# Performance work log

Hardware: AMD Instinct MI355X
Metric: run time of the kernel (lower is better)

The kernel has to match this reference:

```python
import jax, jax.numpy as jnp
import numpy as np

NUM_HEADS = 8
WS = 2  # window_size


def setup_inputs() -> dict:
    key = jax.random.key(0)
    k1, k2, k3 = jax.random.split(key, 3)
    B, N, C = 8, 4096, 512
    x = jax.random.normal(k1, (B, N, C), dtype=jnp.float32)
    W_qkv = jax.random.normal(k2, (3 * C, C), dtype=jnp.float32) * 0.02  # nn.Linear weight [out,in], no bias
    W_proj = jax.random.normal(k3, (C, C), dtype=jnp.float32) * 0.02
    b_proj = jnp.zeros((C,), dtype=jnp.float32)
    return {"x": x, "W_qkv": W_qkv, "W_proj": W_proj, "b_proj": b_proj}


def _attn(q, k, v, scale):
    # q,k,v: [..., heads, T, hd]
    logits = jnp.einsum('...qd,...kd->...qk', q, k) * scale
    p = jax.nn.softmax(logits, axis=-1)
    return jnp.einsum('...qk,...kd->...qd', p, v)


def reference(x, W_qkv, W_proj, b_proj):
    B, N, C = x.shape
    H = W = int(N ** 0.5)
    nh, hd = NUM_HEADS, C // NUM_HEADS
    scale = hd ** -0.5

    # ---- hi branch: avg-pool then global attention on pooled tokens ----
    x_img = x.reshape(B, H, W, C)
    x_hi = x_img.reshape(B, H // WS, WS, W // WS, WS, C).mean(axis=(2, 4))  # [B,Hh,Wh,C]
    Hh, Wh = H // WS, W // WS
    N_hi = Hh * Wh
    x_hi = x_hi.reshape(B, N_hi, C)

    qkv_hi = (x_hi @ W_qkv.T).reshape(B, N_hi, 3, nh, hd).transpose(2, 0, 3, 1, 4)
    out_hi = _attn(qkv_hi[0], qkv_hi[1], qkv_hi[2], scale)          # [B,nh,N_hi,hd]
    out_hi = out_hi.transpose(0, 2, 1, 3).reshape(B, N_hi, C)

    # bilinear upsample (align_corners=False == half-pixel, matches jax.image.resize)
    hi_img = out_hi.reshape(B, Hh, Wh, C).transpose(0, 3, 1, 2)      # [B,C,Hh,Wh]
    hi_up = jax.image.resize(hi_img, (B, C, H, W), method='bilinear')
    out_hi = hi_up.reshape(B, C, N).transpose(0, 2, 1)               # [B,N,C]

    # ---- lo branch: windowed attention (replicating torch unfold layout) ----
    # torch: x.unfold(1,ws,ws).unfold(2,ws,ws) -> [B,Hh,Wh,C,ws,ws]; then
    # .reshape(B,-1,ws*ws,C) reinterprets the contiguous [C,ws,ws] block as [ws*ws,C].
    wnd = x_img.reshape(B, Hh, WS, Wh, WS, C).transpose(0, 1, 3, 5, 2, 4)  # [B,Hh,Wh,C,ws,ws]
    nW = Hh * Wh
    T = WS * WS
    windows = wnd.reshape(B, nW, T, C)  # same raw-memory reinterpretation as torch

    qkv_lo = (windows @ W_qkv.T).reshape(B, nW, T, 3, nh, hd).transpose(3, 0, 1, 4, 2, 5)
    out_lo = _attn(qkv_lo[0], qkv_lo[1], qkv_lo[2], scale)           # [B,nW,nh,T,hd]
    out_lo = out_lo.transpose(0, 1, 3, 2, 4).reshape(B, nW, T, C)

    out_lo = out_lo.reshape(B, Hh, Wh, WS, WS, C).transpose(0, 1, 3, 2, 4, 5).reshape(B, N, C)

    out = out_hi + out_lo
    out = out @ W_proj.T + b_proj
    return out
```

## Files before the change

kernel.cpp:

```cpp
#include <hip/hip_runtime.h>
#include <stdint.h>

typedef unsigned short u16b;
typedef short s16x8 __attribute__((ext_vector_type(8)));
typedef unsigned short u16x4 __attribute__((ext_vector_type(4)));
typedef float f32x4 __attribute__((ext_vector_type(4)));

__device__ __forceinline__ u16b f2bf(float f) {
    uint32_t u = __float_as_uint(f);
    uint32_t r = (u + 0x7FFFu + ((u >> 16) & 1u)) >> 16;
    return (u16b)r;
}
__device__ __forceinline__ u16b f2bf_fast(float f) {
    return (u16b)((__float_as_uint(f) + 0x8000u) >> 16);
}
__device__ __forceinline__ float bf2f(u16b h) {
    return __uint_as_float(((uint32_t)h) << 16);
}

typedef const __attribute__((address_space(1))) void* gas_ptr;
typedef __attribute__((address_space(3))) void* las_ptr;
__device__ __forceinline__ void gload_lds16(const void* g, void* l) {
    __builtin_amdgcn_global_load_lds((gas_ptr)g, (las_ptr)l, 16, 0, 0);
}

__global__ void cast_weights(const float* __restrict__ wqkv, const float* __restrict__ wproj,
                             u16b* __restrict__ wqkv_bf, u16b* __restrict__ wproj_bf) {
    int i = blockIdx.x * 256 + threadIdx.x;
    if (i < 1536 * 512) wqkv_bf[i] = f2bf(wqkv[i]);
    if (i < 512 * 512) wproj_bf[i] = f2bf(wproj[i]);
}

__global__ __launch_bounds__(256) void pool_pack(const float* __restrict__ x,
                                                 u16b* __restrict__ x_hi,
                                                 u16b* __restrict__ xw) {
    int i = blockIdx.x * 256 + threadIdx.x;
    int c4 = i & 127;
    int t = i >> 7;
    int wj = t & 31, wi = (t >> 5) & 31, b = t >> 10;
    const float* p00 = x + ((size_t)b * 4096 + (size_t)(wi * 2) * 64 + wj * 2) * 512 + c4 * 4;
    f32x4 v00 = *(const f32x4*)p00;
    f32x4 v01 = *(const f32x4*)(p00 + 512);
    f32x4 v10 = *(const f32x4*)(p00 + 64 * 512);
    f32x4 v11 = *(const f32x4*)(p00 + 65 * 512);

    u16b ph[4];
#pragma unroll
    for (int j = 0; j < 4; ++j)
        ph[j] = f2bf((v00[j] + v01[j] + v10[j] + v11[j]) * 0.25f);
    *(u16x4*)(x_hi + (size_t)t * 512 + c4 * 4) = *(u16x4*)ph;

    u16b pk[16];
#pragma unroll
    for (int j = 0; j < 4; ++j) {
        pk[j * 4 + 0] = f2bf(v00[j]);
        pk[j * 4 + 1] = f2bf(v01[j]);
        pk[j * 4 + 2] = f2bf(v10[j]);
        pk[j * 4 + 3] = f2bf(v11[j]);
    }
    u16b* dst = xw + ((size_t)t * 4 + (c4 >> 5)) * 512 + (c4 & 31) * 16;
    *(s16x8*)dst = *(s16x8*)pk;
    *(s16x8*)(dst + 8) = *(s16x8*)(pk + 8);
}


template <int RT>
__device__ __forceinline__ void stage_region(const u16b* gsrc, int K, u16b* lds,
                                             int wv, int ldrow, int ldk) {
#pragma unroll
    for (int j = 0; j < 2; ++j) {
        int c = j * 8 + wv;
        int chunk;
        if (RT == 0)      chunk = c + ((c >> 3) << 3);
        else if (RT == 1) chunk = c + ((c >> 3) << 3) + 8;
        else if (RT == 2) chunk = ((c >> 2) << 3) + (c & 3);
        else              chunk = ((c >> 2) << 3) + (c & 3) + 4;
        gload_lds16(gsrc + (size_t)(chunk * 8 + ldrow) * K + ldk, lds + chunk * 512);
    }
}

template <int MH, int NH, int LOADB>
__device__ __forceinline__ void ds_quad(const u16b* Asb, const u16b* Bsb,
                                        int gm, int gn, int l15, int fsw0, int fsw1,
                                        s16x8 (&af)[4][2], s16x8 (&bf)[2][2]) {
#pragma unroll
    for (int i = 0; i < 4; ++i) {
        const u16b* p = Asb + (gm * 128 + (MH * 4 + i) * 16 + l15) * 64;
        af[i][0] = *(const s16x8*)(p + fsw0);
        af[i][1] = *(const s16x8*)(p + fsw1);
    }
    if (LOADB) {
#pragma unroll
        for (int i = 0; i < 2; ++i) {
            const u16b* p = Bsb + (gn * 64 + (NH * 2 + i) * 16 + l15) * 64;
            bf[i][0] = *(const s16x8*)(p + fsw0);
            bf[i][1] = *(const s16x8*)(p + fsw1);
        }
    }
}

template <int MH, int NH>
__device__ __forceinline__ void mfma_quad(s16x8 (&af)[4][2], s16x8 (&bf)[2][2], f32x4 (&acc)[8][4]) {
    __builtin_amdgcn_s_setprio(1);
#pragma unroll
    for (int ks = 0; ks < 2; ++ks)
#pragma unroll
        for (int i = 0; i < 4; ++i)
#pragma unroll
            for (int j = 0; j < 2; ++j)
                acc[MH * 4 + i][NH * 2 + j] = __builtin_amdgcn_mfma_f32_16x16x32_bf16(
                    af[i][ks], bf[j][ks], acc[MH * 4 + i][NH * 2 + j], 0, 0, 0);
    __builtin_amdgcn_s_setprio(0);
}

template <int OUT_F32>
__global__ __launch_bounds__(512, 2) void gemm8(const u16b* __restrict__ A, const u16b* __restrict__ Bt,
                                                u16b* __restrict__ Cbf, float* __restrict__ Cf,
                                                const float* __restrict__ bias, int M, int Nn, int K,
                                                int NB) {
    __shared__ u16b As[2][256 * 64];
    __shared__ u16b Bs[2][256 * 64];
    int tid = threadIdx.x;
    int wv = tid >> 6, lane = tid & 63;
    int quad = lane >> 4, l15 = lane & 15;
    int gm = wv >> 2, gn = wv & 3;

    int nwg = gridDim.x, bid = blockIdx.x;
    int swz = (bid & 7) * (nwg >> 3) + (bid >> 3);
    int nb = swz % NB, mb = swz / NB;
    int m0 = mb * 256, n0 = nb * 256;
    const u16b* Ap = A + (size_t)m0 * K;
    const u16b* Btp = Bt + (size_t)n0 * K;

    int ldrow = lane >> 3;
    int ldk = ((lane & 7) ^ ldrow) * 8;
    int fsw0 = (quad ^ (l15 & 7)) * 8;
    int fsw1 = ((4 + quad) ^ (l15 & 7)) * 8;

    f32x4 acc[8][4] = {};
    s16x8 af[4][2], bf[2][2];
    int nt = K >> 6;

#pragma unroll
    for (int r = 0; r < 4; ++r) {
        int chunk = r * 8 + wv;
        gload_lds16(Ap + (size_t)(chunk * 8 + ldrow) * K + ldk, &As[0][0] + chunk * 512);
    }
#pragma unroll
    for (int r = 0; r < 4; ++r) {
        int chunk = r * 8 + wv;
        gload_lds16(Btp + (size_t)(chunk * 8 + ldrow) * K + ldk, &Bs[0][0] + chunk * 512);
    }
    stage_region<2>(Btp + 64, K, &Bs[1][0], wv, ldrow, ldk);
    stage_region<0>(Ap + 64, K, &As[1][0], wv, ldrow, ldk);
    asm volatile("s_waitcnt vmcnt(4)" ::: "memory");
    __builtin_amdgcn_s_barrier();

    for (int t0 = 0; t0 < nt; t0 += 2) {
        bool s2 = (t0 + 2) < nt;
        bool s3 = (t0 + 3) < nt;
        ds_quad<0, 0, 1>(&As[0][0], &Bs[0][0], gm, gn, l15, fsw0, fsw1, af, bf);
        stage_region<3>(Btp + (size_t)(t0 + 1) * 64, K, &Bs[1][0], wv, ldrow, ldk);
        __builtin_amdgcn_s_barrier();
        mfma_quad<0, 0>(af, bf, acc);
        __builtin_amdgcn_s_barrier();
        ds_quad<1, 0, 0>(&As[0][0], &Bs[0][0], gm, gn, l15, fsw0, fsw1, af, bf);
        stage_region<1>(Ap + (size_t)(t0 + 1) * 64, K, &As[1][0], wv, ldrow, ldk);
        __builtin_amdgcn_s_barrier();
        mfma_quad<1, 0>(af, bf, acc);
        __builtin_amdgcn_s_barrier();
        ds_quad<0, 1, 1>(&As[0][0], &Bs[0][0], gm, gn, l15, fsw0, fsw1, af, bf);
        if (s2) stage_region<2>(Btp + (size_t)(t0 + 2) * 64, K, &Bs[0][0], wv, ldrow, ldk);
        __builtin_amdgcn_s_barrier();
        mfma_quad<0, 1>(af, bf, acc);
        __builtin_amdgcn_s_barrier();
        ds_quad<1, 1, 0>(&As[0][0], &Bs[0][0], gm, gn, l15, fsw0, fsw1, af, bf);
        if (s2) stage_region<0>(Ap + (size_t)(t0 + 2) * 64, K, &As[0][0], wv, ldrow, ldk);
        __builtin_amdgcn_s_barrier();
        mfma_quad<1, 1>(af, bf, acc);
        if (s2) { asm volatile("s_waitcnt vmcnt(4)" ::: "memory"); }
        else    { asm volatile("s_waitcnt vmcnt(0)" ::: "memory"); }
        __builtin_amdgcn_s_barrier();
        ds_quad<0, 0, 1>(&As[1][0], &Bs[1][0], gm, gn, l15, fsw0, fsw1, af, bf);
        if (s2) stage_region<3>(Btp + (size_t)(t0 + 2) * 64, K, &Bs[0][0], wv, ldrow, ldk);
        __builtin_amdgcn_s_barrier();
        mfma_quad<0, 0>(af, bf, acc);
        __builtin_amdgcn_s_barrier();
        ds_quad<1, 0, 0>(&As[1][0], &Bs[1][0], gm, gn, l15, fsw0, fsw1, af, bf);
        if (s2) stage_region<1>(Ap + (size_t)(t0 + 2) * 64, K, &As[0][0], wv, ldrow, ldk);
        __builtin_amdgcn_s_barrier();
        mfma_quad<1, 0>(af, bf, acc);
        __builtin_amdgcn_s_barrier();
        ds_quad<0, 1, 1>(&As[1][0], &Bs[1][0], gm, gn, l15, fsw0, fsw1, af, bf);
        if (s3) stage_region<2>(Btp + (size_t)(t0 + 3) * 64, K, &Bs[1][0], wv, ldrow, ldk);
        __builtin_amdgcn_s_barrier();
        mfma_quad<0, 1>(af, bf, acc);
        __builtin_amdgcn_s_barrier();
        ds_quad<1, 1, 0>(&As[1][0], &Bs[1][0], gm, gn, l15, fsw0, fsw1, af, bf);
        if (s3) stage_region<0>(Ap + (size_t)(t0 + 3) * 64, K, &As[1][0], wv, ldrow, ldk);
        __builtin_amdgcn_s_barrier();
        mfma_quad<1, 1>(af, bf, acc);
        if (s3) { asm volatile("s_waitcnt vmcnt(4)" ::: "memory"); }
        else    { asm volatile("s_waitcnt vmcnt(0)" ::: "memory"); }
        __builtin_amdgcn_s_barrier();
    }

#pragma unroll
    for (int mi = 0; mi < 8; ++mi)
#pragma unroll
        for (int ni = 0; ni < 4; ++ni) {
            int row = m0 + gm * 128 + mi * 16 + quad * 4;
            int col = n0 + gn * 64 + ni * 16 + l15;
            if (OUT_F32) {
                float bv = bias[col];
#pragma unroll
                for (int r = 0; r < 4; ++r)
                    Cf[(size_t)(row + r) * Nn + col] = acc[mi][ni][r] + bv;
            } else {
#pragma unroll
                for (int r = 0; r < 4; ++r)
                    Cbf[(size_t)(row + r) * Nn + col] = f2bf(acc[mi][ni][r]);
            }
        }
}

__global__ __launch_bounds__(256) void transpose_v(const u16b* __restrict__ qkv, u16b* __restrict__ vt) {
    __shared__ u16b tile[64 * 72];
    int bh = blockIdx.y, nt = blockIdx.x;
    int b = bh >> 3, h = bh & 7;
    int tid = threadIdx.x;
    int row = tid >> 2, part = tid & 3;
    const u16b* src = qkv + ((size_t)b * 1024 + nt * 64 + row) * 1536 + 1024 + h * 64 + part * 16;
    *(s16x8*)&tile[row * 72 + part * 16] = *(const s16x8*)src;
    *(s16x8*)&tile[row * 72 + part * 16 + 8] = *(const s16x8*)(src + 8);
    __syncthreads();
    u16b* dst = vt + ((size_t)bh * 64 + row) * 1024 + nt * 64 + part * 16;
#pragma unroll
    for (int j = 0; j < 16; ++j) dst[j] = tile[(part * 16 + j) * 72 + row];
}

__global__ __launch_bounds__(256) void attn_hi(const u16b* __restrict__ qkv,
                                               const u16b* __restrict__ vt,
                                               u16b* __restrict__ out_hi) {
    __shared__ u16b Ks[2][64 * 64];
    __shared__ u16b Vs[2][64 * 64];
    __shared__ u16b P[4][16 * 64];
    int tid = threadIdx.x, wave = tid >> 6, lane = tid & 63;
    int quad = lane >> 4, l15 = lane & 15;
    int bh = blockIdx.x;
    int qb = blockIdx.y;
    int b = bh >> 3, h = bh & 7;
    int qr0 = qb * 64 + wave * 16;

    const size_t qkv_b = (size_t)b * 1024 * 1536;
    const u16b* kg = qkv + qkv_b + 512 + h * 64;
    const u16b* vg = vt + (size_t)bh * 64 * 1024;

    int srow8 = lane >> 3;
    int ssw = ((lane & 7) ^ srow8) * 8;
    int fsw0 = (quad ^ (l15 & 7)) * 8;
    int fsw1 = ((4 + quad) ^ (l15 & 7)) * 8;

    s16x8 qf[2];
    qf[0] = *(const s16x8*)(qkv + qkv_b + (size_t)(qr0 + l15) * 1536 + h * 64 + quad * 8);
    qf[1] = *(const s16x8*)(qkv + qkv_b + (size_t)(qr0 + l15) * 1536 + h * 64 + 32 + quad * 8);

#pragma unroll
    for (int i = 0; i < 2; ++i) {
        int chunk = wave * 2 + i;
        int row = chunk * 8 + srow8;
        gload_lds16(kg + (size_t)row * 1536 + ssw, (u16b*)Ks[0] + chunk * 512);
        gload_lds16(vg + (size_t)row * 1024 + ssw, (u16b*)Vs[0] + chunk * 512);
    }

    f32x4 o[4] = {};
    f32x4 ls = {0.f, 0.f, 0.f, 0.f};
    u16b* pl = P[wave];
    const float c_scale = 0.18033688011f;

    for (int kb = 0; kb < 16; ++kb) {
        int cur = kb & 1, nxt = cur ^ 1;
        __syncthreads();
        if (kb < 15) {
#pragma unroll
            for (int i = 0; i < 2; ++i) {
                int chunk = wave * 2 + i;
                int row = chunk * 8 + srow8;
                gload_lds16(kg + (size_t)((kb + 1) * 64 + row) * 1536 + ssw, (u16b*)Ks[nxt] + chunk * 512);
                gload_lds16(vg + (size_t)row * 1024 + (kb + 1) * 64 + ssw, (u16b*)Vs[nxt] + chunk * 512);
            }
        }
        const u16b* Kc = Ks[cur];
        const u16b* Vc = Vs[cur];

        f32x4 s[4] = {};
#pragma unroll
        for (int nt = 0; nt < 4; ++nt) {
            s16x8 kf0 = *(const s16x8*)(Kc + (nt * 16 + l15) * 64 + fsw0);
            s16x8 kf1 = *(const s16x8*)(Kc + (nt * 16 + l15) * 64 + fsw1);
            s[nt] = __builtin_amdgcn_mfma_f32_16x16x32_bf16(qf[0], kf0, s[nt], 0, 0, 0);
            s[nt] = __builtin_amdgcn_mfma_f32_16x16x32_bf16(qf[1], kf1, s[nt], 0, 0, 0);
        }
#pragma unroll
        for (int nt = 0; nt < 4; ++nt) {
            f32x4 p;
#pragma unroll
            for (int r = 0; r < 4; ++r) p[r] = exp2f(s[nt][r] * c_scale);
            ls += p;
#pragma unroll
            for (int r = 0; r < 4; ++r) {
                int prow = quad * 4 + r;
                int slc = (nt * 2 + (l15 >> 3)) ^ (prow & 7);
                pl[prow * 64 + slc * 8 + (l15 & 7)] = f2bf_fast(p[r]);
            }
        }
        s16x8 pa0 = *(const s16x8*)(pl + l15 * 64 + fsw0);
        s16x8 pa1 = *(const s16x8*)(pl + l15 * 64 + fsw1);
#pragma unroll
        for (int nd = 0; nd < 4; ++nd) {
            s16x8 vf0 = *(const s16x8*)(Vc + (nd * 16 + l15) * 64 + fsw0);
            s16x8 vf1 = *(const s16x8*)(Vc + (nd * 16 + l15) * 64 + fsw1);
            o[nd] = __builtin_amdgcn_mfma_f32_16x16x32_bf16(pa0, vf0, o[nd], 0, 0, 0);
            o[nd] = __builtin_amdgcn_mfma_f32_16x16x32_bf16(pa1, vf1, o[nd], 0, 0, 0);
        }
    }

    float rs[4];
#pragma unroll
    for (int r = 0; r < 4; ++r) {
        float t = ls[r];
#pragma unroll
        for (int msk = 1; msk < 16; msk <<= 1) t += __shfl_xor(t, msk);
        rs[r] = 1.f / t;
    }
#pragma unroll
    for (int nd = 0; nd < 4; ++nd)
#pragma unroll
        for (int r = 0; r < 4; ++r) {
            int row = qr0 + quad * 4 + r;
            int col = h * 64 + nd * 16 + l15;
            out_hi[((size_t)b * 1024 + row) * 512 + col] = f2bf(o[nd][r] * rs[r]);
        }
}

__global__ __launch_bounds__(256) void attn_lo_up(const u16b* __restrict__ qkv_lo,
                                                  const u16b* __restrict__ out_hi,
                                                  u16b* __restrict__ attn_sum) {
    int tid = threadIdx.x, wave = tid >> 6, lane = tid & 63;
    int wg = blockIdx.x * 4 + wave;
    int h = wg & 7, w = (wg >> 3) & 1023, b = wg >> 13;
    size_t base = ((size_t)(b * 1024 + w) * 4) * 1536 + h * 64 + lane;
    float q[4], k[4], v[4];
#pragma unroll
    for (int t = 0; t < 4; ++t) {
        q[t] = bf2f(qkv_lo[base + t * 1536]);
        k[t] = bf2f(qkv_lo[base + t * 1536 + 512]);
        v[t] = bf2f(qkv_lo[base + t * 1536 + 1024]);
    }
    float lg[4][4];
#pragma unroll
    for (int tq = 0; tq < 4; ++tq)
#pragma unroll
        for (int tk = 0; tk < 4; ++tk) {
            float d = q[tq] * k[tk];
#pragma unroll
            for (int msk = 1; msk < 64; msk <<= 1) d += __shfl_xor(d, msk);
            lg[tq][tk] = d * 0.125f;
        }
    int wi = w >> 5, wj = w & 31;
    const u16b* hsrc = out_hi + (size_t)b * 1024 * 512 + h * 64 + lane;
#pragma unroll
    for (int tq = 0; tq < 4; ++tq) {
        float mx = fmaxf(fmaxf(lg[tq][0], lg[tq][1]), fmaxf(lg[tq][2], lg[tq][3]));
        float p[4], s = 0.f;
#pragma unroll
        for (int tk = 0; tk < 4; ++tk) { p[tk] = exp2f((lg[tq][tk] - mx) * 1.44269504f); s += p[tk]; }
        float ov = 0.f;
#pragma unroll
        for (int tk = 0; tk < 4; ++tk) ov += p[tk] * v[tk];
        ov /= s;
        int py = tq >> 1, px = tq & 1;
        int y0, y1, x0, x1;
        float wy0, wx0;
        if (py == 0) { y0 = wi > 0 ? wi - 1 : 0; y1 = wi; wy0 = 0.25f; }
        else         { y0 = wi; y1 = wi < 31 ? wi + 1 : 31; wy0 = 0.75f; }
        if (px == 0) { x0 = wj > 0 ? wj - 1 : 0; x1 = wj; wx0 = 0.25f; }
        else         { x0 = wj; x1 = wj < 31 ? wj + 1 : 31; wx0 = 0.75f; }
        float wy1 = 1.f - wy0, wx1 = 1.f - wx0;
        float vu = wy0 * (wx0 * bf2f(hsrc[(size_t)(y0 * 32 + x0) * 512]) + wx1 * bf2f(hsrc[(size_t)(y0 * 32 + x1) * 512]))
                 + wy1 * (wx0 * bf2f(hsrc[(size_t)(y1 * 32 + x0) * 512]) + wx1 * bf2f(hsrc[(size_t)(y1 * 32 + x1) * 512]));
        int n = (wi * 2 + py) * 64 + wj * 2 + px;
        attn_sum[((size_t)b * 4096 + n) * 512 + h * 64 + lane] = f2bf(ov + vu);
    }
}

extern "C" void kernel_launch(void* const* d_in, const int* in_sizes, int n_in,
                              void* d_out, int out_size, void* d_ws, size_t ws_size,
                              hipStream_t stream) {
    (void)in_sizes; (void)n_in; (void)out_size; (void)ws_size;
    const float* x = (const float*)d_in[0];
    const float* Wqkv = (const float*)d_in[1];
    const float* Wproj = (const float*)d_in[2];
    const float* bproj = (const float*)d_in[3];
    float* out = (float*)d_out;

    char* ws = (char*)d_ws;
    size_t off = 0;
    auto alloc = [&](size_t bytes) { void* p = ws + off; off += bytes; return p; };
    u16b* wqkv_bf = (u16b*)alloc((size_t)1536 * 512 * 2);
    u16b* wproj_bf = (u16b*)alloc((size_t)512 * 512 * 2);
    u16b* x_hi    = (u16b*)alloc((size_t)8 * 1024 * 512 * 2);
    u16b* xw      = (u16b*)alloc((size_t)8 * 1024 * 4 * 512 * 2);
    u16b* qkv_hi  = (u16b*)alloc((size_t)8 * 1024 * 1536 * 2);
    u16b* qkv_lo  = (u16b*)alloc((size_t)8 * 4096 * 1536 * 2);
    u16b* vt      = (u16b*)alloc((size_t)64 * 64 * 1024 * 2);
    u16b* out_hi  = (u16b*)alloc((size_t)8 * 1024 * 512 * 2);
    u16b* attn_sum= (u16b*)alloc((size_t)8 * 4096 * 512 * 2);

    cast_weights<<<dim3(3072), dim3(256), 0, stream>>>(Wqkv, Wproj, wqkv_bf, wproj_bf);
    pool_pack<<<dim3(4096), dim3(256), 0, stream>>>(x, x_hi, xw);
    gemm8<0><<<dim3(192), dim3(512), 0, stream>>>(x_hi, wqkv_bf, qkv_hi, nullptr, nullptr, 8192, 1536, 512, 6);
    gemm8<0><<<dim3(768), dim3(512), 0, stream>>>(xw, wqkv_bf, qkv_lo, nullptr, nullptr, 32768, 1536, 512, 6);
    transpose_v<<<dim3(16, 64), dim3(256), 0, stream>>>(qkv_hi, vt);
    attn_hi<<<dim3(64, 16), dim3(256), 0, stream>>>(qkv_hi, vt, out_hi);
    attn_lo_up<<<dim3(16384), dim3(256), 0, stream>>>(qkv_lo, out_hi, attn_sum);
    gemm8<1><<<dim3(256), dim3(512), 0, stream>>>(attn_sum, wproj_bf, nullptr, out, bproj, 32768, 512, 512, 2);
}
```

Measured before the change: 356.2 us.

## Use MFMA for windowed attention logits and reorder GEMM quadrant traversal

```diff
diff --git a/kernel.cpp b/kernel.cpp
--- a/kernel.cpp
+++ b/kernel.cpp
@@ -79,17 +79,19 @@
     }
 }
 
-template <int MH, int NH, int LOADB>
+template <int MH, int NH, int LA, int LB>
 __device__ __forceinline__ void ds_quad(const u16b* Asb, const u16b* Bsb,
                                         int gm, int gn, int l15, int fsw0, int fsw1,
                                         s16x8 (&af)[4][2], s16x8 (&bf)[2][2]) {
-#pragma unroll
-    for (int i = 0; i < 4; ++i) {
-        const u16b* p = Asb + (gm * 128 + (MH * 4 + i) * 16 + l15) * 64;
-        af[i][0] = *(const s16x8*)(p + fsw0);
-        af[i][1] = *(const s16x8*)(p + fsw1);
-    }
-    if (LOADB) {
+    if (LA) {
+#pragma unroll
+        for (int i = 0; i < 4; ++i) {
+            const u16b* p = Asb + (gm * 128 + (MH * 4 + i) * 16 + l15) * 64;
+            af[i][0] = *(const s16x8*)(p + fsw0);
+            af[i][1] = *(const s16x8*)(p + fsw1);
+        }
+    }
+    if (LB) {
 #pragma unroll
         for (int i = 0; i < 2; ++i) {
             const u16b* p = Bsb + (gn * 64 + (NH * 2 + i) * 16 + l15) * 64;
@@ -151,55 +153,55 @@
         int chunk = r * 8 + wv;
         gload_lds16(Btp + (size_t)(chunk * 8 + ldrow) * K + ldk, &Bs[0][0] + chunk * 512);
     }
-    stage_region<2>(Btp + 64, K, &Bs[1][0], wv, ldrow, ldk);
     stage_region<0>(Ap + 64, K, &As[1][0], wv, ldrow, ldk);
+    stage_region<3>(Btp + 64, K, &Bs[1][0], wv, ldrow, ldk);
     asm volatile("s_waitcnt vmcnt(4)" ::: "memory");
     __builtin_amdgcn_s_barrier();
 
     for (int t0 = 0; t0 < nt; t0 += 2) {
         bool s2 = (t0 + 2) < nt;
         bool s3 = (t0 + 3) < nt;
-        ds_quad<0, 0, 1>(&As[0][0], &Bs[0][0], gm, gn, l15, fsw0, fsw1, af, bf);
-        stage_region<3>(Btp + (size_t)(t0 + 1) * 64, K, &Bs[1][0], wv, ldrow, ldk);
+        ds_quad<0, 0, 1, 1>(&As[0][0], &Bs[0][0], gm, gn, l15, fsw0, fsw1, af, bf);
+        stage_region<1>(Ap + (size_t)(t0 + 1) * 64, K, &As[1][0], wv, ldrow, ldk);
         __builtin_amdgcn_s_barrier();
         mfma_quad<0, 0>(af, bf, acc);
         __builtin_amdgcn_s_barrier();
-        ds_quad<1, 0, 0>(&As[0][0], &Bs[0][0], gm, gn, l15, fsw0, fsw1, af, bf);
-        stage_region<1>(Ap + (size_t)(t0 + 1) * 64, K, &As[1][0], wv, ldrow, ldk);
+        ds_quad<0, 1, 0, 1>(&As[0][0], &Bs[0][0], gm, gn, l15, fsw0, fsw1, af, bf);
+        stage_region<2>(Btp + (size_t)(t0 + 1) * 64, K, &Bs[1][0], wv, ldrow, ldk);
+        __builtin_amdgcn_s_barrier();
+        mfma_quad<0, 1>(af, bf, acc);
+        __builtin_amdgcn_s_barrier();
+        ds_quad<1, 1, 1, 0>(&As[0][0], &Bs[0][0], gm, gn, l15, fsw0, fsw1, af, bf);
+        if (s2) stage_region<0>(Ap + (size_t)(t0 + 2) * 64, K, &As[0][0], wv, ldrow, ldk);
+        __builtin_amdgcn_s_barrier();
+        mfma_quad<1, 1>(af, bf, acc);
+        __builtin_amdgcn_s_barrier();
+        ds_quad<1, 0, 0, 1>(&As[0][0], &Bs[0][0], gm, gn, l15, fsw0, fsw1, af, bf);
+        if (s2) stage_region<3>(Btp + (size_t)(t0 + 2) * 64, K, &Bs[0][0], wv, ldrow, ldk);
         __builtin_amdgcn_s_barrier();
         mfma_quad<1, 0>(af, bf, acc);
-        __builtin_amdgcn_s_barrier();
-        ds_quad<0, 1, 1>(&As[0][0], &Bs[0][0], gm, gn, l15, fsw0, fsw1, af, bf);
-        if (s2) stage_region<2>(Btp + (size_t)(t0 + 2) * 64, K, &Bs[0][0], wv, ldrow, ldk);
-        __builtin_amdgcn_s_barrier();
-        mfma_quad<0, 1>(af, bf, acc);
-        __builtin_amdgcn_s_barrier();
-        ds_quad<1, 1, 0>(&As[0][0], &Bs[0][0], gm, gn, l15, fsw0, fsw1, af, bf);
-        if (s2) stage_region<0>(Ap + (size_t)(t0 + 2) * 64, K, &As[0][0], wv, ldrow, ldk);
-        __builtin_amdgcn_s_barrier();
-        mfma_quad<1, 1>(af, bf, acc);
         if (s2) { asm volatile("s_waitcnt vmcnt(4)" ::: "memory"); }
         else    { asm volatile("s_waitcnt vmcnt(0)" ::: "memory"); }
         __builtin_amdgcn_s_barrier();
-        ds_quad<0, 0, 1>(&As[1][0], &Bs[1][0], gm, gn, l15, fsw0, fsw1, af, bf);
-        if (s2) stage_region<3>(Btp + (size_t)(t0 + 2) * 64, K, &Bs[0][0], wv, ldrow, ldk);
+        ds_quad<0, 0, 1, 1>(&As[1][0], &Bs[1][0], gm, gn, l15, fsw0, fsw1, af, bf);
+        if (s2) stage_region<1>(Ap + (size_t)(t0 + 2) * 64, K, &As[0][0], wv, ldrow, ldk);
         __builtin_amdgcn_s_barrier();
         mfma_quad<0, 0>(af, bf, acc);
         __builtin_amdgcn_s_barrier();
-        ds_quad<1, 0, 0>(&As[1][0], &Bs[1][0], gm, gn, l15, fsw0, fsw1, af, bf);
-        if (s2) stage_region<1>(Ap + (size_t)(t0 + 2) * 64, K, &As[0][0], wv, ldrow, ldk);
+        ds_quad<0, 1, 0, 1>(&As[1][0], &Bs[1][0], gm, gn, l15, fsw0, fsw1, af, bf);
+        if (s2) stage_region<2>(Btp + (size_t)(t0 + 2) * 64, K, &Bs[0][0], wv, ldrow, ldk);
+        __builtin_amdgcn_s_barrier();
+        mfma_quad<0, 1>(af, bf, acc);
+        __builtin_amdgcn_s_barrier();
+        ds_quad<1, 1, 1, 0>(&As[1][0], &Bs[1][0], gm, gn, l15, fsw0, fsw1, af, bf);
+        if (s3) stage_region<0>(Ap + (size_t)(t0 + 3) * 64, K, &As[1][0], wv, ldrow, ldk);
+        __builtin_amdgcn_s_barrier();
+        mfma_quad<1, 1>(af, bf, acc);
+        __builtin_amdgcn_s_barrier();
+        ds_quad<1, 0, 0, 1>(&As[1][0], &Bs[1][0], gm, gn, l15, fsw0, fsw1, af, bf);
+        if (s3) stage_region<3>(Btp + (size_t)(t0 + 3) * 64, K, &Bs[1][0], wv, ldrow, ldk);
         __builtin_amdgcn_s_barrier();
         mfma_quad<1, 0>(af, bf, acc);
-        __builtin_amdgcn_s_barrier();
-        ds_quad<0, 1, 1>(&As[1][0], &Bs[1][0], gm, gn, l15, fsw0, fsw1, af, bf);
-        if (s3) stage_region<2>(Btp + (size_t)(t0 + 3) * 64, K, &Bs[1][0], wv, ldrow, ldk);
-        __builtin_amdgcn_s_barrier();
-        mfma_quad<0, 1>(af, bf, acc);
-        __builtin_amdgcn_s_barrier();
-        ds_quad<1, 1, 0>(&As[1][0], &Bs[1][0], gm, gn, l15, fsw0, fsw1, af, bf);
-        if (s3) stage_region<0>(Ap + (size_t)(t0 + 3) * 64, K, &As[1][0], wv, ldrow, ldk);
-        __builtin_amdgcn_s_barrier();
-        mfma_quad<1, 1>(af, bf, acc);
         if (s3) { asm volatile("s_waitcnt vmcnt(4)" ::: "memory"); }
         else    { asm volatile("s_waitcnt vmcnt(0)" ::: "memory"); }
         __builtin_amdgcn_s_barrier();
@@ -346,51 +348,73 @@
 __global__ __launch_bounds__(256) void attn_lo_up(const u16b* __restrict__ qkv_lo,
                                                   const u16b* __restrict__ out_hi,
                                                   u16b* __restrict__ attn_sum) {
+    __shared__ float P[4][64];
     int tid = threadIdx.x, wave = tid >> 6, lane = tid & 63;
+    int quad = lane >> 4, l15 = lane & 15;
     int wg = blockIdx.x * 4 + wave;
-    int h = wg & 7, w = (wg >> 3) & 1023, b = wg >> 13;
-    size_t base = ((size_t)(b * 1024 + w) * 4) * 1536 + h * 64 + lane;
-    float q[4], k[4], v[4];
-#pragma unroll
-    for (int t = 0; t < 4; ++t) {
-        q[t] = bf2f(qkv_lo[base + t * 1536]);
-        k[t] = bf2f(qkv_lo[base + t * 1536 + 512]);
-        v[t] = bf2f(qkv_lo[base + t * 1536 + 1024]);
-    }
-    float lg[4][4];
-#pragma unroll
-    for (int tq = 0; tq < 4; ++tq)
-#pragma unroll
-        for (int tk = 0; tk < 4; ++tk) {
-            float d = q[tq] * k[tk];
-#pragma unroll
-            for (int msk = 1; msk < 64; msk <<= 1) d += __shfl_xor(d, msk);
-            lg[tq][tk] = d * 0.125f;
-        }
+    int h = wg & 7, w4 = (wg >> 3) & 255, b = wg >> 11;
+    int w0 = w4 * 4;
+
+    const u16b* qb = qkv_lo + ((size_t)(b * 1024 + w0 + (l15 >> 2)) * 4 + (l15 & 3)) * 1536 + h * 64 + quad * 8;
+    s16x8 qf0 = *(const s16x8*)qb;
+    s16x8 qf1 = *(const s16x8*)(qb + 32);
+    s16x8 kf0 = *(const s16x8*)(qb + 512);
+    s16x8 kf1 = *(const s16x8*)(qb + 544);
+    f32x4 s = {};
+    s = __builtin_amdgcn_mfma_f32_16x16x32_bf16(qf0, kf0, s, 0, 0, 0);
+    s = __builtin_amdgcn_mfma_f32_16x16x32_bf16(qf1, kf1, s, 0, 0, 0);
+    bool valid = (l15 >> 2) == quad;
+    float* pl = &P[wave][quad * 16];
+#pragma unroll
+    for (int r = 0; r < 4; ++r) {
+        float v = s[r] * 0.125f;
+        float m = fmaxf(v, __shfl_xor(v, 1));
+        m = fmaxf(m, __shfl_xor(m, 2));
+        float e = exp2f((v - m) * 1.44269504f);
+        float sm = e + __shfl_xor(e, 1);
+        sm += __shfl_xor(sm, 2);
+        if (valid) pl[r * 4 + (l15 & 3)] = e / sm;
+    }
+
+    int win = quad, d4 = l15 * 4;
+    int w = w0 + win;
     int wi = w >> 5, wj = w & 31;
-    const u16b* hsrc = out_hi + (size_t)b * 1024 * 512 + h * 64 + lane;
+    const u16b* vb = qkv_lo + ((size_t)(b * 1024 + w) * 4) * 1536 + 1024 + h * 64 + d4;
+    float vf[4][4];
+#pragma unroll
+    for (int tk = 0; tk < 4; ++tk) {
+        u16x4 vv = *(const u16x4*)(vb + (size_t)tk * 1536);
+#pragma unroll
+        for (int j = 0; j < 4; ++j) vf[tk][j] = bf2f(vv[j]);
+    }
+    int rr[3] = { wi > 0 ? wi - 1 : 0, wi, wi < 31 ? wi + 1 : 31 };
+    int cc[3] = { wj > 0 ? wj - 1 : 0, wj, wj < 31 ? wj + 1 : 31 };
+    float hv[3][3][4];
+    const u16b* hb = out_hi + (size_t)b * 1024 * 512 + h * 64 + d4;
+#pragma unroll
+    for (int iy = 0; iy < 3; ++iy)
+#pragma unroll
+        for (int ix = 0; ix < 3; ++ix) {
+            u16x4 t = *(const u16x4*)(hb + (size_t)(rr[iy] * 32 + cc[ix]) * 512);
+#pragma unroll
+            for (int j = 0; j < 4; ++j) hv[iy][ix][j] = bf2f(t[j]);
+        }
 #pragma unroll
     for (int tq = 0; tq < 4; ++tq) {
-        float mx = fmaxf(fmaxf(lg[tq][0], lg[tq][1]), fmaxf(lg[tq][2], lg[tq][3]));
-        float p[4], s = 0.f;
-#pragma unroll
-        for (int tk = 0; tk < 4; ++tk) { p[tk] = exp2f((lg[tq][tk] - mx) * 1.44269504f); s += p[tk]; }
-        float ov = 0.f;
-#pragma unroll
-        for (int tk = 0; tk < 4; ++tk) ov += p[tk] * v[tk];
-        ov /= s;
+        f32x4 pq = *(const f32x4*)&P[wave][win * 16 + tq * 4];
         int py = tq >> 1, px = tq & 1;
-        int y0, y1, x0, x1;
-        float wy0, wx0;
-        if (py == 0) { y0 = wi > 0 ? wi - 1 : 0; y1 = wi; wy0 = 0.25f; }
-        else         { y0 = wi; y1 = wi < 31 ? wi + 1 : 31; wy0 = 0.75f; }
-        if (px == 0) { x0 = wj > 0 ? wj - 1 : 0; x1 = wj; wx0 = 0.25f; }
-        else         { x0 = wj; x1 = wj < 31 ? wj + 1 : 31; wx0 = 0.75f; }
+        float wy0 = py ? 0.75f : 0.25f, wx0 = px ? 0.75f : 0.25f;
         float wy1 = 1.f - wy0, wx1 = 1.f - wx0;
-        float vu = wy0 * (wx0 * bf2f(hsrc[(size_t)(y0 * 32 + x0) * 512]) + wx1 * bf2f(hsrc[(size_t)(y0 * 32 + x1) * 512]))
-                 + wy1 * (wx0 * bf2f(hsrc[(size_t)(y1 * 32 + x0) * 512]) + wx1 * bf2f(hsrc[(size_t)(y1 * 32 + x1) * 512]));
+        u16b ov[4];
+#pragma unroll
+        for (int j = 0; j < 4; ++j) {
+            float o = pq[0] * vf[0][j] + pq[1] * vf[1][j] + pq[2] * vf[2][j] + pq[3] * vf[3][j];
+            float vu = wy0 * (wx0 * hv[py][px][j] + wx1 * hv[py][px + 1][j])
+                     + wy1 * (wx0 * hv[py + 1][px][j] + wx1 * hv[py + 1][px + 1][j]);
+            ov[j] = f2bf(o + vu);
+        }
         int n = (wi * 2 + py) * 64 + wj * 2 + px;
-        attn_sum[((size_t)b * 4096 + n) * 512 + h * 64 + lane] = f2bf(ov + vu);
+        *(u16x4*)(attn_sum + ((size_t)(b * 4096 + n)) * 512 + h * 64 + d4) = *(u16x4*)ov;
     }
 }
 
@@ -423,6 +447,6 @@
     gemm8<0><<<dim3(768), dim3(512), 0, stream>>>(xw, wqkv_bf, qkv_lo, nullptr, nullptr, 32768, 1536, 512, 6);
     transpose_v<<<dim3(16, 64), dim3(256), 0, stream>>>(qkv_hi, vt);
     attn_hi<<<dim3(64, 16), dim3(256), 0, stream>>>(qkv_hi, vt, out_hi);
-    attn_lo_up<<<dim3(16384), dim3(256), 0, stream>>>(qkv_lo, out_hi, attn_sum);
+    attn_lo_up<<<dim3(4096), dim3(256), 0, stream>>>(qkv_lo, out_hi, attn_sum);
     gemm8<1><<<dim3(256), dim3(512), 0, stream>>>(attn_sum, wproj_bf, nullptr, out, bproj, 32768, 512, 512, 2);
 }
```

Result: faster. 313.0 us (-12.1%).
